# Performance work log

Measured on AMD Instinct MI355X. Metric: run time of the kernel, lower is better.

The kernel has to match this reference:

```python
import jax, jax.numpy as jnp
import numpy as np

BSZ, T, H, P, N = 2, 2048, 16, 64, 64

def setup_inputs() -> dict:
    key = jax.random.key(0)
    k1, k2, k3, k4, k5 = jax.random.split(key, 5)
    X = jax.random.normal(k1, (BSZ, T, H, P), dtype=jnp.float32)
    delta = jax.random.uniform(k2, (BSZ, T, H), dtype=jnp.float32)
    Bmat = jax.random.normal(k3, (BSZ, T, N), dtype=jnp.float32)
    Cmat = jax.random.normal(k4, (BSZ, T, N), dtype=jnp.float32)
    # module init: A_log = log(arange(1, n_heads+1))
    A_log = jnp.log(jnp.arange(1, H + 1, dtype=jnp.float32))
    return {"X": X, "delta": delta, "Bmat": Bmat, "Cmat": Cmat, "A_log": A_log}

def reference(X, delta, Bmat, Cmat, A_log):
    # X: [B,T,H,P], delta: [B,T,H], Bmat/Cmat: [B,T,N], A_log: [H]
    Bsz, Tlen, Hh, Pp = X.shape
    Nn = Bmat.shape[-1]
    dA = jnp.exp(delta * -jnp.exp(A_log))  # [B,T,H] per-step scalar decay

    def step(h, inp):
        dA_t, dt_t, X_t, B_t, C_t = inp  # [B,H], [B,H], [B,H,P], [B,N], [B,N]
        # outer-product input: delta * X outer B -> [B,H,P,N]
        dBx = (dt_t[:, :, None, None] * X_t[..., None]) * B_t[:, None, None, :]
        h = dA_t[:, :, None, None] * h + dBx
        y_t = jnp.einsum('bhpn,bn->bhp', h, C_t)
        return h, y_t

    h0 = jnp.zeros((Bsz, Hh, Pp, Nn), dtype=X.dtype)
    xs = (
        jnp.moveaxis(dA, 1, 0),    # [T,B,H]
        jnp.moveaxis(delta, 1, 0), # [T,B,H]
        jnp.moveaxis(X, 1, 0),     # [T,B,H,P]
        jnp.moveaxis(Bmat, 1, 0),  # [T,B,N]
        jnp.moveaxis(Cmat, 1, 0),  # [T,B,N]
    )
    h_last, ys = jax.lax.scan(step, h0, xs)
    y = jnp.moveaxis(ys, 0, 1)  # [B,T,H,P]
    return y, h_last
```

## Files before the change

### kernel.cpp

```cpp
#include <hip/hip_runtime.h>


constexpr int BSZ = 2, T = 2048, H = 16, P = 64, N = 64;
constexpr int L = 64, NC = T / L;
constexpr int HB = 4, NHB = H / HB;
constexpr int LS = 72;

using bf16x8 = __attribute__((ext_vector_type(8))) short;
using f32x4  = __attribute__((ext_vector_type(4))) float;

__device__ inline ushort f2bf(float f) {
    unsigned u = __float_as_uint(f);
    u += 0x7FFFu + ((u >> 16) & 1u);
    return (ushort)(u >> 16);
}
__device__ inline unsigned pack2(float a, float b) {
    return (unsigned)f2bf(a) | ((unsigned)f2bf(b) << 16);
}
__device__ inline float bf2f(ushort h) {
    return __uint_as_float(((unsigned)h) << 16);
}

__global__ __launch_bounds__(256, 1) void p1_intra(
    const float* __restrict__ X, const float* __restrict__ delta,
    const float* __restrict__ Bm, const float* __restrict__ Cm,
    const float* __restrict__ A_log,
    float* __restrict__ Y, float* __restrict__ Hbuf, float* __restrict__ Dchunk)
{
    __shared__ __align__(16) ushort sB [64 * LS];
    __shared__ __align__(16) ushort sC [64 * LS];
    __shared__ __align__(16) ushort sBt[64 * LS];
    __shared__ __align__(16) ushort sXt[HB][64 * LS];
    __shared__ __align__(16) ushort sS [HB][64 * LS];
    __shared__ float sSa[HB][64], sSb[HB][64], sW[HB][64];

    const int tid  = threadIdx.x, lane = tid & 63, w = tid >> 6;
    const int quad = lane >> 4,   l16  = lane & 15;
    const int blk = blockIdx.x;
    const int hg  = blk & (NHB - 1);
    const int c   = (blk >> 2) & (NC - 1);
    const int b   = blk >> 7;
    const int h   = hg * HB + w;
    const int t0  = c * L;
    const int chunkid = (b * H + h) * NC + c;

    {
        const float4* gB4 = (const float4*)(Bm + ((size_t)b * T + t0) * N);
        const float4* gC4 = (const float4*)(Cm + ((size_t)b * T + t0) * N);
        #pragma unroll
        for (int r = 0; r < 4; ++r) {
            int idx = r * 256 + tid;
            int t = idx >> 4, n4 = (idx & 15) << 2;
            float4 vb = gB4[idx], vc = gC4[idx];
            *(uint2*)&sB[t * LS + n4] = make_uint2(pack2(vb.x, vb.y), pack2(vb.z, vb.w));
            *(uint2*)&sC[t * LS + n4] = make_uint2(pack2(vc.x, vc.y), pack2(vc.z, vc.w));
        }
    }
    {
        const float* gB = Bm + ((size_t)b * T + t0) * N;
        #pragma unroll
        for (int i = 0; i < 8; ++i) {
            int tau = (w * 8 + i) * 2;
            float v0 = gB[(size_t)tau * N + lane];
            float v1 = gB[(size_t)(tau + 1) * N + lane];
            *(unsigned*)&sBt[lane * LS + tau] = pack2(v0, v1);
        }
    }
    {
        const float* gX = X + (((size_t)b * T + t0) * H + h) * P;
        #pragma unroll 8
        for (int i = 0; i < 32; ++i) {
            float v0 = gX[(size_t)(2 * i)     * (H * P) + lane];
            float v1 = gX[(size_t)(2 * i + 1) * (H * P) + lane];
            *(unsigned*)&sXt[w][lane * LS + 2 * i] = pack2(v0, v1);
        }
    }
    const float negA = -__expf(A_log[h]);
    {
        float dl = delta[((size_t)b * T + t0 + lane) * H + h];
        float s = negA * dl;
        #pragma unroll
        for (int off = 1; off < 64; off <<= 1) {
            float u = __shfl_up(s, off, 64);
            if (lane >= off) s += u;
        }
        float sL  = __shfl(s, 63, 64);
        float lnd = __logf(dl);
        sSa[w][lane] = s;
        sSb[w][lane] = lnd - s;
        sW [w][lane] = __expf(sL + lnd - s);
        if (lane == 63) Dchunk[chunkid] = __expf(sL);
    }
    __syncthreads();

    f32x4 g[4][4];
    #pragma unroll
    for (int i = 0; i < 4; ++i)
        #pragma unroll
        for (int j = 0; j < 4; ++j) g[i][j] = (f32x4){0.f, 0.f, 0.f, 0.f};
    #pragma unroll
    for (int ks = 0; ks < 2; ++ks) {
        const int ko = ks * 32 + quad * 8;
        bf16x8 af[4], bfr[4];
        #pragma unroll
        for (int i = 0; i < 4; ++i) af[i]  = *(const bf16x8*)&sC[(i * 16 + l16) * LS + ko];
        #pragma unroll
        for (int j = 0; j < 4; ++j) bfr[j] = *(const bf16x8*)&sB[(j * 16 + l16) * LS + ko];
        #pragma unroll
        for (int i = 0; i < 4; ++i)
            #pragma unroll
            for (int j = 0; j < 4; ++j)
                g[i][j] = __builtin_amdgcn_mfma_f32_16x16x32_bf16(af[i], bfr[j], g[i][j], 0, 0, 0);
    }

    #pragma unroll
    for (int jt = 0; jt < 4; ++jt) {
        const int tau = jt * 16 + l16;
        const float sb = sSb[w][tau];
        #pragma unroll
        for (int it = 0; it < 4; ++it) {
            #pragma unroll
            for (int r = 0; r < 4; ++r) {
                const int t = it * 16 + quad * 4 + r;
                float arg = (tau <= t) ? (sSa[w][t] + sb) : -80.0f;
                float sv = __expf(arg) * g[it][jt][r];
                sS[w][t * LS + tau] = f2bf(sv);
            }
        }
    }
    __syncthreads();

    f32x4 ya[4][4], ha[4][4];
    #pragma unroll
    for (int i = 0; i < 4; ++i)
        #pragma unroll
        for (int j = 0; j < 4; ++j) {
            ya[i][j] = (f32x4){0.f, 0.f, 0.f, 0.f};
            ha[i][j] = (f32x4){0.f, 0.f, 0.f, 0.f};
        }
    #pragma unroll
    for (int ks = 0; ks < 2; ++ks) {
        const int ko = ks * 32 + quad * 8;
        bf16x8 sa[4], xb[4], bb[4], xw[4];
        #pragma unroll
        for (int i = 0; i < 4; ++i) sa[i] = *(const bf16x8*)&sS [w][(i * 16 + l16) * LS + ko];
        #pragma unroll
        for (int i = 0; i < 4; ++i) xb[i] = *(const bf16x8*)&sXt[w][(i * 16 + l16) * LS + ko];
        #pragma unroll
        for (int i = 0; i < 4; ++i) bb[i] = *(const bf16x8*)&sBt[(i * 16 + l16) * LS + ko];
        float wv[8];
        #pragma unroll
        for (int j = 0; j < 8; ++j) wv[j] = sW[w][ko + j];
        #pragma unroll
        for (int i = 0; i < 4; ++i)
            #pragma unroll
            for (int j = 0; j < 8; ++j)
                xw[i][j] = (short)f2bf(bf2f((ushort)xb[i][j]) * wv[j]);
        #pragma unroll
        for (int it = 0; it < 4; ++it)
            #pragma unroll
            for (int jt = 0; jt < 4; ++jt)
                ya[it][jt] = __builtin_amdgcn_mfma_f32_16x16x32_bf16(sa[it], xb[jt], ya[it][jt], 0, 0, 0);
        #pragma unroll
        for (int ip = 0; ip < 4; ++ip)
            #pragma unroll
            for (int jn = 0; jn < 4; ++jn)
                ha[ip][jn] = __builtin_amdgcn_mfma_f32_16x16x32_bf16(xw[ip], bb[jn], ha[ip][jn], 0, 0, 0);
    }

    float* Yg = Y + (((size_t)b * T + t0) * H + h) * P;
    #pragma unroll
    for (int it = 0; it < 4; ++it)
        #pragma unroll
        for (int jt = 0; jt < 4; ++jt)
            #pragma unroll
            for (int r = 0; r < 4; ++r)
                Yg[(size_t)(it * 16 + quad * 4 + r) * (H * P) + jt * 16 + l16] = ya[it][jt][r];
    float* Hg = Hbuf + (size_t)chunkid * (P * N);
    #pragma unroll
    for (int ip = 0; ip < 4; ++ip)
        #pragma unroll
        for (int jn = 0; jn < 4; ++jn)
            #pragma unroll
            for (int r = 0; r < 4; ++r)
                Hg[(ip * 16 + quad * 4 + r) * N + jn * 16 + l16] = ha[ip][jn][r];
}

__global__ __launch_bounds__(256) void p2_scan(
    const float* __restrict__ Dchunk, float* __restrict__ Hbuf,
    float* __restrict__ Hlast)
{
    const int idx = blockIdx.x * 256 + threadIdx.x;
    const int bh = idx >> 10, e4 = idx & 1023;
    float4* H4 = (float4*)Hbuf;
    float4 hs = {0.f, 0.f, 0.f, 0.f};
    #pragma unroll 4
    for (int c = 0; c < NC; ++c) {
        const size_t off = ((size_t)(bh * NC + c) << 10) + e4;
        float4 tmp = H4[off];
        float D = Dchunk[bh * NC + c];
        H4[off] = hs;
        hs.x = D * hs.x + tmp.x;
        hs.y = D * hs.y + tmp.y;
        hs.z = D * hs.z + tmp.z;
        hs.w = D * hs.w + tmp.w;
    }
    ((float4*)Hlast)[idx] = hs;
}

__global__ __launch_bounds__(256, 1) void p3_inter(
    const float* __restrict__ delta, const float* __restrict__ Cm,
    const float* __restrict__ A_log, const float* __restrict__ Hbuf,
    float* __restrict__ Y)
{
    __shared__ __align__(16) ushort sC[64 * LS];
    __shared__ __align__(16) ushort sH[HB][64 * LS];
    __shared__ float sLam[HB][64];

    const int tid  = threadIdx.x, lane = tid & 63, w = tid >> 6;
    const int quad = lane >> 4,   l16  = lane & 15;
    const int blk = blockIdx.x;
    const int hg  = blk & (NHB - 1);
    const int c   = (blk >> 2) & (NC - 1);
    const int b   = blk >> 7;
    const int h   = hg * HB + w;
    const int t0  = c * L;
    const int chunkid = (b * H + h) * NC + c;

    {
        const float4* gC4 = (const float4*)(Cm + ((size_t)b * T + t0) * N);
        #pragma unroll
        for (int r = 0; r < 4; ++r) {
            int idx = r * 256 + tid;
            int t = idx >> 4, n4 = (idx & 15) << 2;
            float4 vc = gC4[idx];
            *(uint2*)&sC[t * LS + n4] = make_uint2(pack2(vc.x, vc.y), pack2(vc.z, vc.w));
        }
    }
    {
        float dl = delta[((size_t)b * T + t0 + lane) * H + h];
        float s = -__expf(A_log[h]) * dl;
        #pragma unroll
        for (int off = 1; off < 64; off <<= 1) {
            float u = __shfl_up(s, off, 64);
            if (lane >= off) s += u;
        }
        sLam[w][lane] = __expf(s);
    }
    {
        const float4* Hg4 = (const float4*)(Hbuf + (size_t)chunkid * (P * N));
        #pragma unroll
        for (int i = 0; i < 16; ++i) {
            int idx = i * 64 + lane;
            float4 v = Hg4[idx];
            int p = idx >> 4, n4 = (idx & 15) << 2;
            *(uint2*)&sH[w][p * LS + n4] = make_uint2(pack2(v.x, v.y), pack2(v.z, v.w));
        }
    }
    __syncthreads();

    f32x4 acc[4][4];
    #pragma unroll
    for (int i = 0; i < 4; ++i)
        #pragma unroll
        for (int j = 0; j < 4; ++j) acc[i][j] = (f32x4){0.f, 0.f, 0.f, 0.f};
    #pragma unroll
    for (int ks = 0; ks < 2; ++ks) {
        const int ko = ks * 32 + quad * 8;
        bf16x8 ca[4], hb[4];
        #pragma unroll
        for (int i = 0; i < 4; ++i) ca[i] = *(const bf16x8*)&sC[(i * 16 + l16) * LS + ko];
        #pragma unroll
        for (int j = 0; j < 4; ++j) hb[j] = *(const bf16x8*)&sH[w][(j * 16 + l16) * LS + ko];
        #pragma unroll
        for (int it = 0; it < 4; ++it)
            #pragma unroll
            for (int jp = 0; jp < 4; ++jp)
                acc[it][jp] = __builtin_amdgcn_mfma_f32_16x16x32_bf16(ca[it], hb[jp], acc[it][jp], 0, 0, 0);
    }

    float* Yg = Y + (((size_t)b * T + t0) * H + h) * P;
    #pragma unroll
    for (int it = 0; it < 4; ++it)
        #pragma unroll
        for (int jp = 0; jp < 4; ++jp)
            #pragma unroll
            for (int r = 0; r < 4; ++r) {
                const int t = it * 16 + quad * 4 + r;
                const size_t off = (size_t)t * (H * P) + jp * 16 + l16;
                Yg[off] = Yg[off] + sLam[w][t] * acc[it][jp][r];
            }
}

extern "C" void kernel_launch(void* const* d_in, const int* in_sizes, int n_in,
                              void* d_out, int out_size, void* d_ws, size_t ws_size,
                              hipStream_t stream) {
    const float* X     = (const float*)d_in[0];
    const float* delta = (const float*)d_in[1];
    const float* Bm    = (const float*)d_in[2];
    const float* Cm    = (const float*)d_in[3];
    const float* A_log = (const float*)d_in[4];

    float* Y     = (float*)d_out;
    float* Hlast = (float*)d_out + (size_t)BSZ * T * H * P;

    float* Hbuf   = (float*)d_ws;
    float* Dchunk = (float*)d_ws + (size_t)BSZ * H * NC * P * N;

    const int nblk = BSZ * NC * NHB;
    p1_intra<<<nblk, 256, 0, stream>>>(X, delta, Bm, Cm, A_log, Y, Hbuf, Dchunk);
    p2_scan<<<(BSZ * H * P * N / 4) / 256, 256, 0, stream>>>(Dchunk, Hbuf, Hlast);
    p3_inter<<<nblk, 256, 0, stream>>>(delta, Cm, A_log, Hbuf, Y);
}
```

Measured before the change: 107.6 us.

## Assign one head per block and split chunk rows across waves

The intra-chunk and inter-chunk kernels now map each block to a single (batch, chunk, head) instead of four heads, with the four waves each owning 16 time rows. This gives 4x more blocks, smaller per-wave register tiles and less shared memory, so occupancy can rise (launch bounds raised). The chunk scan kernel switches to scalar-per-thread with all chunk states loaded into registers up front, giving more threads and more loads in flight. The cost is that B/C loads and the Bt transpose are now repeated per head rather than shared by four heads.

Result: faster. 103.3 us (-4.0%).

```diff
diff --git a/kernel.cpp b/kernel.cpp
--- a/kernel.cpp
+++ b/kernel.cpp
@@ -3,7 +3,6 @@
 
 constexpr int BSZ = 2, T = 2048, H = 16, P = 64, N = 64;
 constexpr int L = 64, NC = T / L;
-constexpr int HB = 4, NHB = H / HB;
 constexpr int LS = 72;
 
 using bf16x8 = __attribute__((ext_vector_type(8))) short;
@@ -21,7 +20,7 @@
     return __uint_as_float(((unsigned)h) << 16);
 }
 
-__global__ __launch_bounds__(256, 1) void p1_intra(
+__global__ __launch_bounds__(256, 3) void p1_intra(
     const float* __restrict__ X, const float* __restrict__ delta,
     const float* __restrict__ Bm, const float* __restrict__ Cm,
     const float* __restrict__ A_log,
@@ -30,17 +29,16 @@
     __shared__ __align__(16) ushort sB [64 * LS];
     __shared__ __align__(16) ushort sC [64 * LS];
     __shared__ __align__(16) ushort sBt[64 * LS];
-    __shared__ __align__(16) ushort sXt[HB][64 * LS];
-    __shared__ __align__(16) ushort sS [HB][64 * LS];
-    __shared__ float sSa[HB][64], sSb[HB][64], sW[HB][64];
+    __shared__ __align__(16) ushort sXt[64 * LS];
+    __shared__ __align__(16) ushort sS [64 * LS];
+    __shared__ float sSa[64], sSb[64], sW[64];
 
     const int tid  = threadIdx.x, lane = tid & 63, w = tid >> 6;
     const int quad = lane >> 4,   l16  = lane & 15;
     const int blk = blockIdx.x;
-    const int hg  = blk & (NHB - 1);
-    const int c   = (blk >> 2) & (NC - 1);
-    const int b   = blk >> 7;
-    const int h   = hg * HB + w;
+    const int h   = blk & (H - 1);
+    const int c   = (blk >> 4) & (NC - 1);
+    const int b   = blk >> 9;
     const int t0  = c * L;
     const int chunkid = (b * H + h) * NC + c;
 
@@ -49,8 +47,7 @@
         const float4* gC4 = (const float4*)(Cm + ((size_t)b * T + t0) * N);
         #pragma unroll
         for (int r = 0; r < 4; ++r) {
-            int idx = r * 256 + tid;
-            int t = idx >> 4, n4 = (idx & 15) << 2;
+            int idx = r * 256 + tid, t = idx >> 4, n4 = (idx & 15) << 2;
             float4 vb = gB4[idx], vc = gC4[idx];
             *(uint2*)&sB[t * LS + n4] = make_uint2(pack2(vb.x, vb.y), pack2(vb.z, vb.w));
             *(uint2*)&sC[t * LS + n4] = make_uint2(pack2(vc.x, vc.y), pack2(vc.z, vc.w));
@@ -68,17 +65,17 @@
     }
     {
         const float* gX = X + (((size_t)b * T + t0) * H + h) * P;
-        #pragma unroll 8
-        for (int i = 0; i < 32; ++i) {
-            float v0 = gX[(size_t)(2 * i)     * (H * P) + lane];
-            float v1 = gX[(size_t)(2 * i + 1) * (H * P) + lane];
-            *(unsigned*)&sXt[w][lane * LS + 2 * i] = pack2(v0, v1);
-        }
-    }
-    const float negA = -__expf(A_log[h]);
-    {
+        #pragma unroll
+        for (int i = 0; i < 8; ++i) {
+            int tau = w * 16 + 2 * i;
+            float v0 = gX[(size_t)tau * (H * P) + lane];
+            float v1 = gX[(size_t)(tau + 1) * (H * P) + lane];
+            *(unsigned*)&sXt[lane * LS + tau] = pack2(v0, v1);
+        }
+    }
+    if (w == 0) {
         float dl = delta[((size_t)b * T + t0 + lane) * H + h];
-        float s = negA * dl;
+        float s = -__expf(A_log[h]) * dl;
         #pragma unroll
         for (int off = 1; off < 64; off <<= 1) {
             float u = __shfl_up(s, off, 64);
@@ -86,158 +83,134 @@
         }
         float sL  = __shfl(s, 63, 64);
         float lnd = __logf(dl);
-        sSa[w][lane] = s;
-        sSb[w][lane] = lnd - s;
-        sW [w][lane] = __expf(sL + lnd - s);
+        sSa[lane] = s;
+        sSb[lane] = lnd - s;
+        sW [lane] = __expf(sL + lnd - s);
         if (lane == 63) Dchunk[chunkid] = __expf(sL);
     }
     __syncthreads();
 
-    f32x4 g[4][4];
-    #pragma unroll
-    for (int i = 0; i < 4; ++i)
-        #pragma unroll
-        for (int j = 0; j < 4; ++j) g[i][j] = (f32x4){0.f, 0.f, 0.f, 0.f};
+    f32x4 g[4];
+    #pragma unroll
+    for (int j = 0; j < 4; ++j) g[j] = (f32x4){0.f, 0.f, 0.f, 0.f};
     #pragma unroll
     for (int ks = 0; ks < 2; ++ks) {
         const int ko = ks * 32 + quad * 8;
-        bf16x8 af[4], bfr[4];
-        #pragma unroll
-        for (int i = 0; i < 4; ++i) af[i]  = *(const bf16x8*)&sC[(i * 16 + l16) * LS + ko];
-        #pragma unroll
-        for (int j = 0; j < 4; ++j) bfr[j] = *(const bf16x8*)&sB[(j * 16 + l16) * LS + ko];
-        #pragma unroll
-        for (int i = 0; i < 4; ++i)
-            #pragma unroll
-            for (int j = 0; j < 4; ++j)
-                g[i][j] = __builtin_amdgcn_mfma_f32_16x16x32_bf16(af[i], bfr[j], g[i][j], 0, 0, 0);
-    }
-
+        bf16x8 af = *(const bf16x8*)&sC[(w * 16 + l16) * LS + ko];
+        #pragma unroll
+        for (int jt = 0; jt < 4; ++jt) {
+            bf16x8 bfr = *(const bf16x8*)&sB[(jt * 16 + l16) * LS + ko];
+            g[jt] = __builtin_amdgcn_mfma_f32_16x16x32_bf16(af, bfr, g[jt], 0, 0, 0);
+        }
+    }
     #pragma unroll
     for (int jt = 0; jt < 4; ++jt) {
         const int tau = jt * 16 + l16;
-        const float sb = sSb[w][tau];
-        #pragma unroll
-        for (int it = 0; it < 4; ++it) {
-            #pragma unroll
-            for (int r = 0; r < 4; ++r) {
-                const int t = it * 16 + quad * 4 + r;
-                float arg = (tau <= t) ? (sSa[w][t] + sb) : -80.0f;
-                float sv = __expf(arg) * g[it][jt][r];
-                sS[w][t * LS + tau] = f2bf(sv);
-            }
+        const float sb = sSb[tau];
+        #pragma unroll
+        for (int r = 0; r < 4; ++r) {
+            const int t = w * 16 + quad * 4 + r;
+            float arg = (tau <= t) ? (sSa[t] + sb) : -80.0f;
+            sS[t * LS + tau] = f2bf(__expf(arg) * g[jt][r]);
         }
     }
     __syncthreads();
 
-    f32x4 ya[4][4], ha[4][4];
-    #pragma unroll
-    for (int i = 0; i < 4; ++i)
-        #pragma unroll
-        for (int j = 0; j < 4; ++j) {
-            ya[i][j] = (f32x4){0.f, 0.f, 0.f, 0.f};
-            ha[i][j] = (f32x4){0.f, 0.f, 0.f, 0.f};
-        }
+    f32x4 ya[4], ha[4];
+    #pragma unroll
+    for (int j = 0; j < 4; ++j) {
+        ya[j] = (f32x4){0.f, 0.f, 0.f, 0.f};
+        ha[j] = (f32x4){0.f, 0.f, 0.f, 0.f};
+    }
     #pragma unroll
     for (int ks = 0; ks < 2; ++ks) {
         const int ko = ks * 32 + quad * 8;
-        bf16x8 sa[4], xb[4], bb[4], xw[4];
-        #pragma unroll
-        for (int i = 0; i < 4; ++i) sa[i] = *(const bf16x8*)&sS [w][(i * 16 + l16) * LS + ko];
-        #pragma unroll
-        for (int i = 0; i < 4; ++i) xb[i] = *(const bf16x8*)&sXt[w][(i * 16 + l16) * LS + ko];
-        #pragma unroll
-        for (int i = 0; i < 4; ++i) bb[i] = *(const bf16x8*)&sBt[(i * 16 + l16) * LS + ko];
-        float wv[8];
-        #pragma unroll
-        for (int j = 0; j < 8; ++j) wv[j] = sW[w][ko + j];
-        #pragma unroll
-        for (int i = 0; i < 4; ++i)
-            #pragma unroll
-            for (int j = 0; j < 8; ++j)
-                xw[i][j] = (short)f2bf(bf2f((ushort)xb[i][j]) * wv[j]);
-        #pragma unroll
-        for (int it = 0; it < 4; ++it)
-            #pragma unroll
-            for (int jt = 0; jt < 4; ++jt)
-                ya[it][jt] = __builtin_amdgcn_mfma_f32_16x16x32_bf16(sa[it], xb[jt], ya[it][jt], 0, 0, 0);
-        #pragma unroll
-        for (int ip = 0; ip < 4; ++ip)
-            #pragma unroll
-            for (int jn = 0; jn < 4; ++jn)
-                ha[ip][jn] = __builtin_amdgcn_mfma_f32_16x16x32_bf16(xw[ip], bb[jn], ha[ip][jn], 0, 0, 0);
+        bf16x8 sa = *(const bf16x8*)&sS [(w * 16 + l16) * LS + ko];
+        bf16x8 xa = *(const bf16x8*)&sXt[(w * 16 + l16) * LS + ko];
+        bf16x8 xw;
+        #pragma unroll
+        for (int j = 0; j < 8; ++j)
+            xw[j] = (short)f2bf(bf2f((ushort)xa[j]) * sW[ko + j]);
+        #pragma unroll
+        for (int jp = 0; jp < 4; ++jp) {
+            bf16x8 xb = *(const bf16x8*)&sXt[(jp * 16 + l16) * LS + ko];
+            ya[jp] = __builtin_amdgcn_mfma_f32_16x16x32_bf16(sa, xb, ya[jp], 0, 0, 0);
+        }
+        #pragma unroll
+        for (int jn = 0; jn < 4; ++jn) {
+            bf16x8 bb = *(const bf16x8*)&sBt[(jn * 16 + l16) * LS + ko];
+            ha[jn] = __builtin_amdgcn_mfma_f32_16x16x32_bf16(xw, bb, ha[jn], 0, 0, 0);
+        }
     }
 
     float* Yg = Y + (((size_t)b * T + t0) * H + h) * P;
     #pragma unroll
-    for (int it = 0; it < 4; ++it)
-        #pragma unroll
-        for (int jt = 0; jt < 4; ++jt)
-            #pragma unroll
-            for (int r = 0; r < 4; ++r)
-                Yg[(size_t)(it * 16 + quad * 4 + r) * (H * P) + jt * 16 + l16] = ya[it][jt][r];
+    for (int jp = 0; jp < 4; ++jp)
+        #pragma unroll
+        for (int r = 0; r < 4; ++r)
+            Yg[(size_t)(w * 16 + quad * 4 + r) * (H * P) + jp * 16 + l16] = ya[jp][r];
     float* Hg = Hbuf + (size_t)chunkid * (P * N);
     #pragma unroll
-    for (int ip = 0; ip < 4; ++ip)
-        #pragma unroll
-        for (int jn = 0; jn < 4; ++jn)
-            #pragma unroll
-            for (int r = 0; r < 4; ++r)
-                Hg[(ip * 16 + quad * 4 + r) * N + jn * 16 + l16] = ha[ip][jn][r];
-}
-
-__global__ __launch_bounds__(256) void p2_scan(
+    for (int jn = 0; jn < 4; ++jn)
+        #pragma unroll
+        for (int r = 0; r < 4; ++r)
+            Hg[(w * 16 + quad * 4 + r) * N + jn * 16 + l16] = ha[jn][r];
+}
+
+__global__ __launch_bounds__(256, 4) void p2_scan(
     const float* __restrict__ Dchunk, float* __restrict__ Hbuf,
     float* __restrict__ Hlast)
 {
-    const int idx = blockIdx.x * 256 + threadIdx.x;
-    const int bh = idx >> 10, e4 = idx & 1023;
-    float4* H4 = (float4*)Hbuf;
-    float4 hs = {0.f, 0.f, 0.f, 0.f};
-    #pragma unroll 4
+    const int bh  = blockIdx.x >> 4;
+    const int rem = ((blockIdx.x & 15) << 8) | threadIdx.x;
+    float v[NC];
+    #pragma unroll
+    for (int c = 0; c < NC; ++c)
+        v[c] = Hbuf[(((size_t)(bh * NC + c)) << 12) + rem];
+    float hs = 0.0f;
+    #pragma unroll
     for (int c = 0; c < NC; ++c) {
-        const size_t off = ((size_t)(bh * NC + c) << 10) + e4;
-        float4 tmp = H4[off];
-        float D = Dchunk[bh * NC + c];
-        H4[off] = hs;
-        hs.x = D * hs.x + tmp.x;
-        hs.y = D * hs.y + tmp.y;
-        hs.z = D * hs.z + tmp.z;
-        hs.w = D * hs.w + tmp.w;
-    }
-    ((float4*)Hlast)[idx] = hs;
-}
-
-__global__ __launch_bounds__(256, 1) void p3_inter(
+        const float tmp = v[c];
+        v[c] = hs;
+        hs = Dchunk[bh * NC + c] * hs + tmp;
+    }
+    #pragma unroll
+    for (int c = 0; c < NC; ++c)
+        Hbuf[(((size_t)(bh * NC + c)) << 12) + rem] = v[c];
+    Hlast[(size_t)bh * 4096 + rem] = hs;
+}
+
+__global__ __launch_bounds__(256, 4) void p3_inter(
     const float* __restrict__ delta, const float* __restrict__ Cm,
     const float* __restrict__ A_log, const float* __restrict__ Hbuf,
     float* __restrict__ Y)
 {
     __shared__ __align__(16) ushort sC[64 * LS];
-    __shared__ __align__(16) ushort sH[HB][64 * LS];
-    __shared__ float sLam[HB][64];
+    __shared__ __align__(16) ushort sH[64 * LS];
+    __shared__ float sLam[64];
 
     const int tid  = threadIdx.x, lane = tid & 63, w = tid >> 6;
     const int quad = lane >> 4,   l16  = lane & 15;
     const int blk = blockIdx.x;
-    const int hg  = blk & (NHB - 1);
-    const int c   = (blk >> 2) & (NC - 1);
-    const int b   = blk >> 7;
-    const int h   = hg * HB + w;
+    const int h   = blk & (H - 1);
+    const int c   = (blk >> 4) & (NC - 1);
+    const int b   = blk >> 9;
     const int t0  = c * L;
     const int chunkid = (b * H + h) * NC + c;
 
     {
         const float4* gC4 = (const float4*)(Cm + ((size_t)b * T + t0) * N);
-        #pragma unroll
-        for (int r = 0; r < 4; ++r) {
-            int idx = r * 256 + tid;
-            int t = idx >> 4, n4 = (idx & 15) << 2;
+        const float4* Hg4 = (const float4*)(Hbuf + (size_t)chunkid * (P * N));
+        #pragma unroll
+        for (int r = 0; r < 4; ++r) {
+            int idx = r * 256 + tid, t = idx >> 4, n4 = (idx & 15) << 2;
             float4 vc = gC4[idx];
+            float4 vh = Hg4[idx];
             *(uint2*)&sC[t * LS + n4] = make_uint2(pack2(vc.x, vc.y), pack2(vc.z, vc.w));
-        }
-    }
-    {
+            *(uint2*)&sH[t * LS + n4] = make_uint2(pack2(vh.x, vh.y), pack2(vh.z, vh.w));
+        }
+    }
+    if (w == 0) {
         float dl = delta[((size_t)b * T + t0 + lane) * H + h];
         float s = -__expf(A_log[h]) * dl;
         #pragma unroll
@@ -245,51 +218,33 @@
             float u = __shfl_up(s, off, 64);
             if (lane >= off) s += u;
         }
-        sLam[w][lane] = __expf(s);
-    }
-    {
-        const float4* Hg4 = (const float4*)(Hbuf + (size_t)chunkid * (P * N));
-        #pragma unroll
-        for (int i = 0; i < 16; ++i) {
-            int idx = i * 64 + lane;
-            float4 v = Hg4[idx];
-            int p = idx >> 4, n4 = (idx & 15) << 2;
-            *(uint2*)&sH[w][p * LS + n4] = make_uint2(pack2(v.x, v.y), pack2(v.z, v.w));
-        }
+        sLam[lane] = __expf(s);
     }
     __syncthreads();
 
-    f32x4 acc[4][4];
-    #pragma unroll
-    for (int i = 0; i < 4; ++i)
-        #pragma unroll
-        for (int j = 0; j < 4; ++j) acc[i][j] = (f32x4){0.f, 0.f, 0.f, 0.f};
+    f32x4 acc[4];
+    #pragma unroll
+    for (int j = 0; j < 4; ++j) acc[j] = (f32x4){0.f, 0.f, 0.f, 0.f};
     #pragma unroll
     for (int ks = 0; ks < 2; ++ks) {
         const int ko = ks * 32 + quad * 8;
-        bf16x8 ca[4], hb[4];
-        #pragma unroll
-        for (int i = 0; i < 4; ++i) ca[i] = *(const bf16x8*)&sC[(i * 16 + l16) * LS + ko];
-        #pragma unroll
-        for (int j = 0; j < 4; ++j) hb[j] = *(const bf16x8*)&sH[w][(j * 16 + l16) * LS + ko];
-        #pragma unroll
-        for (int it = 0; it < 4; ++it)
-            #pragma unroll
-            for (int jp = 0; jp < 4; ++jp)
-                acc[it][jp] = __builtin_amdgcn_mfma_f32_16x16x32_bf16(ca[it], hb[jp], acc[it][jp], 0, 0, 0);
+        bf16x8 ca = *(const bf16x8*)&sC[(w * 16 + l16) * LS + ko];
+        #pragma unroll
+        for (int jp = 0; jp < 4; ++jp) {
+            bf16x8 hb = *(const bf16x8*)&sH[(jp * 16 + l16) * LS + ko];
+            acc[jp] = __builtin_amdgcn_mfma_f32_16x16x32_bf16(ca, hb, acc[jp], 0, 0, 0);
+        }
     }
 
     float* Yg = Y + (((size_t)b * T + t0) * H + h) * P;
     #pragma unroll
-    for (int it = 0; it < 4; ++it)
-        #pragma unroll
-        for (int jp = 0; jp < 4; ++jp)
-            #pragma unroll
-            for (int r = 0; r < 4; ++r) {
-                const int t = it * 16 + quad * 4 + r;
-                const size_t off = (size_t)t * (H * P) + jp * 16 + l16;
-                Yg[off] = Yg[off] + sLam[w][t] * acc[it][jp][r];
-            }
+    for (int jp = 0; jp < 4; ++jp)
+        #pragma unroll
+        for (int r = 0; r < 4; ++r) {
+            const int t = w * 16 + quad * 4 + r;
+            const size_t off = (size_t)t * (H * P) + jp * 16 + l16;
+            Yg[off] = Yg[off] + sLam[t] * acc[jp][r];
+        }
 }
 
 extern "C" void kernel_launch(void* const* d_in, const int* in_sizes, int n_in,
@@ -307,8 +262,8 @@
     float* Hbuf   = (float*)d_ws;
     float* Dchunk = (float*)d_ws + (size_t)BSZ * H * NC * P * N;
 
-    const int nblk = BSZ * NC * NHB;
+    const int nblk = BSZ * NC * H;
     p1_intra<<<nblk, 256, 0, stream>>>(X, delta, Bm, Cm, A_log, Y, Hbuf, Dchunk);
-    p2_scan<<<(BSZ * H * P * N / 4) / 256, 256, 0, stream>>>(Dchunk, Hbuf, Hlast);
+    p2_scan<<<(BSZ * H * P * N) / 256, 256, 0, stream>>>(Dchunk, Hbuf, Hlast);
     p3_inter<<<nblk, 256, 0, stream>>>(delta, Cm, A_log, Hbuf, Y);
 }
```
